# Performance work log

Measured on AMD Instinct MI355X. Metric: run time of the kernel, lower is better.

Reference implementation:

```python
import jax, jax.numpy as jnp
import numpy as np


def setup_inputs() -> dict:
    key = jax.random.key(0)
    k1, k2, k3, k4 = jax.random.split(key, 4)
    d_in, d_out = 1024, 1024
    x = jax.random.normal(k1, (4, 2048, d_in), dtype=jnp.float32)
    # nn.Linear weights, stored as [d_in, d_out] for x @ W (torch stores transpose)
    s = 1.0 / np.sqrt(d_in)
    Wq = jax.random.normal(k2, (d_in, d_out), dtype=jnp.float32) * s
    Wk = jax.random.normal(k3, (d_in, d_out), dtype=jnp.float32) * s
    Wv = jax.random.normal(k4, (d_in, d_out), dtype=jnp.float32) * s
    return {"x": x, "Wq": Wq, "Wk": Wk, "Wv": Wv}


def reference(x, Wq, Wk, Wv):
    # x: [b, s, d_in]; projections (no bias)
    q = jnp.einsum('bsi,io->bso', x, Wq)
    k = jnp.einsum('bsi,io->bso', x, Wk)
    v = jnp.einsum('bsi,io->bso', x, Wv)
    d_out = k.shape[-1]
    scores = jnp.einsum('bqd,bkd->bqk', q, k) / jnp.sqrt(jnp.float32(d_out))
    seq_len = x.shape[1]
    causal = jnp.tril(jnp.ones((seq_len, seq_len), dtype=bool))  # [s, s]
    scores = jnp.where(causal[None, :, :], scores, -jnp.inf)
    weights = jax.nn.softmax(scores, axis=-1)
    return jnp.einsum('bqk,bkd->bqd', weights, v)
```

## Files before the change

kernel.cpp:

```cpp
#include <hip/hip_runtime.h>

typedef __attribute__((ext_vector_type(8))) short bf16x8;
typedef __attribute__((ext_vector_type(4))) float f32x4;
typedef unsigned int u32;

__device__ __forceinline__ unsigned short f2bf(float f) {
  union { float f; unsigned int u; } a; a.f = f;
  unsigned int u = a.u;
  u += 0x7FFFu + ((u >> 16) & 1u);
  return (unsigned short)(u >> 16);
}

__device__ __forceinline__ void gload16(const unsigned short* g, unsigned short* l) {
  __builtin_amdgcn_global_load_lds((const __attribute__((address_space(1))) u32*)g,
                                   (__attribute__((address_space(3))) u32*)l, 16, 0, 0);
}

#define BK 64

template<int MODE>
__global__ __launch_bounds__(256, 4)
void gemm_bt(const unsigned short* __restrict__ A,
             const unsigned short* __restrict__ Bm,
             float* __restrict__ Cf,
             float* __restrict__ Cf2,
             unsigned short* __restrict__ Cb,
             int K, long aBatch, long bBatch, long cBatch, float scale)
{
  constexpr int NI    = (MODE == 0) ? 4 : 2;
  constexpr int TNc   = (MODE == 0) ? 128 : 64;
  constexpr int BROWS = (MODE == 0) ? 32 : 16;
  constexpr int BG    = (MODE == 0) ? 4 : 2;

  int z = blockIdx.z;
  A  += (long)z * aBatch;
  Bm += (long)z * bBatch;
  if (MODE == 2) { Cb += (long)z * cBatch; Cf += (long)z * 2048; }
  if (MODE == 3) { Cf += (long)z * cBatch; Cf2 += (long)z * 2048; }

  int bm0 = 0, bn, p = 0;
  if (MODE == 2) {
    int f = blockIdx.x;
    int r = (int)((sqrtf((float)(4 * f + 1)) - 1.0f) * 0.5f);
    while ((r + 1) * (r + 2) <= f) r++;
    while (r * (r + 1) > f) r--;
    bm0 = r * 128;
    bn  = (f - r * (r + 1)) * 64;
  } else if (MODE == 3) {
    p  = blockIdx.y;
    bn = blockIdx.x * 64;
  } else {
    bm0 = blockIdx.y * 128;
    bn  = blockIdx.x * TNc;
  }

  __shared__ __align__(16) unsigned short As[128 * BK];
  __shared__ __align__(16) unsigned short Bs[TNc * BK];

  int tid  = threadIdx.x;
  int wave = tid >> 6, lane = tid & 63;
  int wm = (MODE == 0) ? (wave >> 1) * 64 : wave * 32;
  int wn = (MODE == 0) ? (wave & 1) * 64 : 0;
  int quad = lane >> 4, l16 = lane & 15;

  int r8 = lane >> 3;
  int c  = (lane & 7) ^ r8;
  const unsigned short* Bg = Bm + (long)(bn + wave * BROWS + r8) * K + c * 8;
  unsigned short* Al = &As[(wave * 32) * BK];
  unsigned short* Bl = &Bs[(wave * BROWS) * BK];

  const int nseg = (MODE == 3) ? 2 : 1;
  for (int seg = 0; seg < nseg; seg++) {
    int bm   = (MODE == 3) ? ((seg == 0) ? (15 - p) * 128 : p * 128) : bm0;
    int Keff = (MODE == 3) ? ((seg == 0) ? 128 * (16 - p) : 128 * (p + 1)) : K;
    const unsigned short* Ag = A + (long)(bm + wave * 32 + r8) * K + c * 8;

    f32x4 acc[NI][4] = {};

    for (int k0 = 0; k0 < Keff; k0 += BK) {
#pragma unroll
      for (int g = 0; g < 4; g++)
        gload16(Ag + k0 + (long)g * 8 * K, Al + g * 8 * BK);
#pragma unroll
      for (int g = 0; g < BG; g++)
        gload16(Bg + k0 + (long)g * 8 * K, Bl + g * 8 * BK);
      __syncthreads();

#pragma unroll
      for (int h = 0; h < 2; h++) {
        bf16x8 af[NI], bfr[4];
#pragma unroll
        for (int i = 0; i < NI; i++)
          af[i]  = *(const bf16x8*)&As[(wm + i * 16 + l16) * BK + (((quad + 4 * h) ^ (l16 & 7)) * 8)];
#pragma unroll
        for (int j = 0; j < 4; j++)
          bfr[j] = *(const bf16x8*)&Bs[(wn + j * 16 + l16) * BK + (((quad + 4 * h) ^ (l16 & 7)) * 8)];
#pragma unroll
        for (int i = 0; i < NI; i++)
#pragma unroll
          for (int j = 0; j < 4; j++)
            acc[i][j] = __builtin_amdgcn_mfma_f32_16x16x32_bf16(af[i], bfr[j], acc[i][j], 0, 0, 0);
      }
      __syncthreads();
    }

#pragma unroll
    for (int i = 0; i < NI; i++) {
      int grow0 = bm + wm + i * 16 + quad * 4;
      if (MODE == 2) {
#pragma unroll
        for (int r = 0; r < 4; r++) {
          int grow = grow0 + r;
          float rowpart = 0.f;
#pragma unroll
          for (int j = 0; j < 4; j++) {
            int gcol = bn + j * 16 + l16;
            float e = (gcol <= grow) ? __expf(acc[i][j][r] * scale) : 0.f;
            rowpart += e;
            Cb[(long)grow * 2048 + gcol] = f2bf(e);
          }
          rowpart += __shfl_xor(rowpart, 1);
          rowpart += __shfl_xor(rowpart, 2);
          rowpart += __shfl_xor(rowpart, 4);
          rowpart += __shfl_xor(rowpart, 8);
          if (l16 == 0) atomicAdd(&Cf[grow], rowpart);
        }
      } else if (MODE == 3) {
        float rinv[4];
#pragma unroll
        for (int r = 0; r < 4; r++) rinv[r] = 1.0f / Cf2[grow0 + r];
#pragma unroll
        for (int j = 0; j < 4; j++) {
          int gcol = bn + j * 16 + l16;
#pragma unroll
          for (int r = 0; r < 4; r++)
            Cf[(long)(grow0 + r) * 1024 + gcol] = acc[i][j][r] * rinv[r];
        }
      } else if (MODE == 1) {
#pragma unroll
        for (int j = 0; j < 4; j++) {
          int gcol = bn + j * 16 + l16;
#pragma unroll
          for (int r = 0; r < 4; r++)
            Cb[(long)(grow0 + r) * 1024 + gcol] = f2bf(acc[i][j][r]);
        }
      } else {
#pragma unroll
        for (int j = 0; j < 4; j++) {
          int gcol = bn + wn + j * 16 + l16;
          int which = gcol >> 10;
          int col = gcol & 1023;
          if (which == 0) {
#pragma unroll
            for (int r = 0; r < 4; r++)
              Cb[(long)(grow0 + r) * 1024 + col] = f2bf(acc[i][j][r]);
          } else {
            unsigned short* Vt = Cb + (long)8192 * 1024;
            int bb = grow0 >> 11, s = grow0 & 2047;
            ushort4 pk;
            pk.x = f2bf(acc[i][j][0]); pk.y = f2bf(acc[i][j][1]);
            pk.z = f2bf(acc[i][j][2]); pk.w = f2bf(acc[i][j][3]);
            *(ushort4*)(Vt + ((long)bb * 1024 + col) * 2048 + s) = pk;
          }
        }
      }
    }
  }
}

__global__ __launch_bounds__(256)
void prep(const float* __restrict__ x,
          const float* __restrict__ W0, const float* __restrict__ W1,
          const float* __restrict__ W2,
          unsigned short* __restrict__ Xb,
          unsigned short* __restrict__ Wqb, unsigned short* __restrict__ Wkb,
          unsigned short* __restrict__ WvT,
          float* __restrict__ rsum)
{
  __shared__ float tile[32][33];
  int b = blockIdx.x;
  if (b < 8192) {
    long i = ((long)b * 256 + threadIdx.x) * 4;
    float4 v = *(const float4*)(x + i);
    ushort4 o;
    o.x = f2bf(v.x); o.y = f2bf(v.y); o.z = f2bf(v.z); o.w = f2bf(v.w);
    *(ushort4*)(Xb + i) = o;
  } else if (b < 10240) {
    int t = b - 8192;
    const float* W    = (t < 1024) ? W0 : W1;
    unsigned short* D = (t < 1024) ? Wqb : Wkb;
    long i = ((long)(t & 1023) * 256 + threadIdx.x) * 4;
    float4 v = *(const float4*)(W + i);
    ushort4 o;
    o.x = f2bf(v.x); o.y = f2bf(v.y); o.z = f2bf(v.z); o.w = f2bf(v.w);
    *(ushort4*)(D + i) = o;
  } else if (b < 11264) {
    int q = b - 10240;
    int kb = (q >> 5) * 32, nb = (q & 31) * 32;
    int tx = threadIdx.x & 31, ty = threadIdx.x >> 5;
    for (int r = ty; r < 32; r += 8)
      tile[r][tx] = W2[(long)(kb + r) * 1024 + nb + tx];
    __syncthreads();
    for (int r = ty; r < 32; r += 8)
      WvT[(long)(nb + r) * 1024 + kb + tx] = f2bf(tile[tx][r]);
  } else {
    long i = ((long)(b - 11264) * 256 + threadIdx.x) * 4;
    float4 zz = {0.f, 0.f, 0.f, 0.f};
    *(float4*)(rsum + i) = zz;
  }
}

extern "C" void kernel_launch(void* const* d_in, const int* in_sizes, int n_in,
                              void* d_out, int out_size, void* d_ws, size_t ws_size,
                              hipStream_t stream) {
  const float* x  = (const float*)d_in[0];
  const float* Wq = (const float*)d_in[1];
  const float* Wk = (const float*)d_in[2];
  const float* Wv = (const float*)d_in[3];
  float* out = (float*)d_out;

  unsigned short* Xb  = (unsigned short*)d_ws;
  unsigned short* Wqb = Xb  + (long)8192 * 1024;
  unsigned short* Wkb = Wqb + (long)1024 * 1024;
  unsigned short* TVB = Wkb + (long)1024 * 1024;
  unsigned short* T   = TVB + (long)2048 * 1024;
  unsigned short* Vt  = T   + (long)8192 * 1024;
  unsigned short* E   = Vt  + (long)8192 * 1024;
  float* rsum         = (float*)(E + (long)4 * 2048 * 2048);

  prep<<<11272, 256, 0, stream>>>(x, Wq, Wk, Wv, Xb, Wqb, Wkb,
                                  TVB + (long)1024 * 1024, rsum);

  gemm_bt<1><<<dim3(16, 8, 1), 256, 0, stream>>>(Wkb, Wqb, nullptr, nullptr, TVB,
      1024, 0, 0, 0, 1.f);

  gemm_bt<0><<<dim3(16, 64, 1), 256, 0, stream>>>(Xb, TVB, nullptr, nullptr, T,
      1024, 0, 0, 0, 1.f);

  gemm_bt<2><<<dim3(272, 1, 4), 256, 0, stream>>>(T, Xb, rsum, nullptr, E, 1024,
      (long)2048 * 1024, (long)2048 * 1024, (long)2048 * 2048, 0.03125f);

  gemm_bt<3><<<dim3(16, 8, 4), 256, 0, stream>>>(E, Vt, out, rsum, nullptr, 2048,
      (long)2048 * 2048, (long)1024 * 2048, (long)2048 * 1024, 1.f);
}
```

Measured before the change: 217.3 us.

## Replace projection GEMM with 256x256-tile, 4-stage pipelined 512-thread kernel

Adds a dedicated gemm_tv kernel for the X·[T|V] projection. It uses 256x256 output tiles with 8 waves, a 4-slot LDS ring of 32-wide K slices prefetched three stages ahead with global_load_lds, explicit vmcnt waits, and setprio around the MFMA block. This replaces the synchronous single-buffered 128x128 gemm_bt<0>. The goal is to hide global-load latency and raise data reuse per tile. The cost is higher register and LDS pressure and a smaller grid of 256 blocks.

```diff
diff --git a/kernel.cpp b/kernel.cpp
--- a/kernel.cpp
+++ b/kernel.cpp
@@ -163,6 +163,102 @@
             *(ushort4*)(Vt + ((long)bb * 1024 + col) * 2048 + s) = pk;
           }
         }
+      }
+    }
+  }
+}
+
+__global__ __launch_bounds__(512, 2)
+void gemm_tv(const unsigned short* __restrict__ A,
+             const unsigned short* __restrict__ Bm,
+             unsigned short* __restrict__ Cb)
+{
+  constexpr int SLICE = 32;
+  constexpr int SLOT  = 256 * SLICE;
+  __shared__ __align__(16) unsigned short As[4 * SLOT];
+  __shared__ __align__(16) unsigned short Bs[4 * SLOT];
+
+  const int tid  = threadIdx.x;
+  const int wave = tid >> 6, lane = tid & 63;
+  const int quad = lane >> 4, l16 = lane & 15;
+  const int bm = blockIdx.y * 256;
+  const int bn = blockIdx.x * 256;
+  const int wm = (wave >> 2) * 128;
+  const int wn = (wave & 3) * 64;
+
+  const int srow = lane >> 2;
+  const int sc   = ((lane & 3) ^ ((lane >> 3) & 3)) * 8;
+  const unsigned short* Ag = A  + (long)(bm + wave * 32 + srow) * 1024 + sc;
+  const unsigned short* Bg = Bm + (long)(bn + wave * 32 + srow) * 1024 + sc;
+  unsigned short* Asl = As + wave * (32 * SLICE);
+  unsigned short* Bsl = Bs + wave * (32 * SLICE);
+
+  const int pc = (quad ^ ((l16 >> 1) & 3)) * 8;
+
+  f32x4 acc[8][4] = {};
+
+#define STAGE(s)                                                          \
+  { const int so_ = ((s) & 3) * SLOT; const int ko_ = (s) * SLICE;        \
+    gload16(Ag + ko_,             Asl + so_);                             \
+    gload16(Ag + ko_ + 16 * 1024, Asl + so_ + 16 * SLICE);                \
+    gload16(Bg + ko_,             Bsl + so_);                             \
+    gload16(Bg + ko_ + 16 * 1024, Bsl + so_ + 16 * SLICE); }
+
+  STAGE(0) STAGE(1) STAGE(2)
+  asm volatile("s_waitcnt vmcnt(8) lgkmcnt(0)" ::: "memory");
+  __builtin_amdgcn_sched_barrier(0);
+  __builtin_amdgcn_s_barrier();
+
+  constexpr int ns = 1024 / SLICE;
+#pragma unroll 1
+  for (int s = 0; s < ns; ++s) {
+    if (s + 3 < ns) STAGE(s + 3)
+    const unsigned short* Asr = As + (s & 3) * SLOT;
+    const unsigned short* Bsr = Bs + (s & 3) * SLOT;
+    bf16x8 af[8], bfr[4];
+#pragma unroll
+    for (int i = 0; i < 8; ++i)
+      af[i]  = *(const bf16x8*)&Asr[(wm + i * 16 + l16) * SLICE + pc];
+#pragma unroll
+    for (int j = 0; j < 4; ++j)
+      bfr[j] = *(const bf16x8*)&Bsr[(wn + j * 16 + l16) * SLICE + pc];
+    __builtin_amdgcn_s_setprio(1);
+#pragma unroll
+    for (int i = 0; i < 8; ++i)
+#pragma unroll
+      for (int j = 0; j < 4; ++j)
+        acc[i][j] = __builtin_amdgcn_mfma_f32_16x16x32_bf16(af[i], bfr[j], acc[i][j], 0, 0, 0);
+    __builtin_amdgcn_s_setprio(0);
+    if (s < ns - 3)
+      asm volatile("s_waitcnt vmcnt(8) lgkmcnt(0)" ::: "memory");
+    else if (s == ns - 3)
+      asm volatile("s_waitcnt vmcnt(4) lgkmcnt(0)" ::: "memory");
+    else
+      asm volatile("s_waitcnt vmcnt(0) lgkmcnt(0)" ::: "memory");
+    __builtin_amdgcn_sched_barrier(0);
+    __builtin_amdgcn_s_barrier();
+  }
+#undef STAGE
+
+#pragma unroll
+  for (int i = 0; i < 8; ++i) {
+    int grow0 = bm + wm + i * 16 + quad * 4;
+#pragma unroll
+    for (int j = 0; j < 4; ++j) {
+      int gcol = bn + wn + j * 16 + l16;
+      int which = gcol >> 10;
+      int col = gcol & 1023;
+      if (which == 0) {
+#pragma unroll
+        for (int r = 0; r < 4; r++)
+          Cb[(long)(grow0 + r) * 1024 + col] = f2bf(acc[i][j][r]);
+      } else {
+        unsigned short* Vt = Cb + (long)8192 * 1024;
+        int bb = grow0 >> 11, ss = grow0 & 2047;
+        ushort4 pk;
+        pk.x = f2bf(acc[i][j][0]); pk.y = f2bf(acc[i][j][1]);
+        pk.z = f2bf(acc[i][j][2]); pk.w = f2bf(acc[i][j][3]);
+        *(ushort4*)(Vt + ((long)bb * 1024 + col) * 2048 + ss) = pk;
       }
     }
   }
@@ -234,8 +330,7 @@
   gemm_bt<1><<<dim3(16, 8, 1), 256, 0, stream>>>(Wkb, Wqb, nullptr, nullptr, TVB,
       1024, 0, 0, 0, 1.f);
 
-  gemm_bt<0><<<dim3(16, 64, 1), 256, 0, stream>>>(Xb, TVB, nullptr, nullptr, T,
-      1024, 0, 0, 0, 1.f);
+  gemm_tv<<<dim3(8, 32, 1), 512, 0, stream>>>(Xb, TVB, T);
 
   gemm_bt<2><<<dim3(272, 1, 4), 256, 0, stream>>>(T, Xb, rsum, nullptr, E, 1024,
       (long)2048 * 1024, (long)2048 * 1024, (long)2048 * 2048, 0.03125f);
```

Measured after the change: 228.3 us. +5.1%, slower.

## Replace T/V projection GEMM with 256x256 double-buffered 8-wave pipelined kernel

Applied to the files above, without the earlier changes.

The MODE 0 path of the generic GEMM, which computes x·[Wk·Wqᵀ | Wv] into T and the transposed V, is replaced by a dedicated kernel. It uses 512 threads, 256x256 output tiles and double-buffered LDS, and issues global loads for the next K-tiles while four phases of MFMAs run, with explicit vmcnt waits, barriers and setprio. The larger tile increases operand reuse per load, and the schedule is meant to hide global-load latency. In exchange it uses 128 KB of LDS per block and launches only 256 blocks, so occupancy is low and the hand-built barrier/waitcnt scheme adds correctness risk.

```diff
diff --git a/kernel.cpp b/kernel.cpp
--- a/kernel.cpp
+++ b/kernel.cpp
@@ -27,10 +27,9 @@
              unsigned short* __restrict__ Cb,
              int K, long aBatch, long bBatch, long cBatch, float scale)
 {
-  constexpr int NI    = (MODE == 0) ? 4 : 2;
-  constexpr int TNc   = (MODE == 0) ? 128 : 64;
-  constexpr int BROWS = (MODE == 0) ? 32 : 16;
-  constexpr int BG    = (MODE == 0) ? 4 : 2;
+  constexpr int NI    = 2;
+  constexpr int BROWS = 16;
+  constexpr int BG    = 2;
 
   int z = blockIdx.z;
   A  += (long)z * aBatch;
@@ -51,16 +50,15 @@
     bn = blockIdx.x * 64;
   } else {
     bm0 = blockIdx.y * 128;
-    bn  = blockIdx.x * TNc;
+    bn  = blockIdx.x * 64;
   }
 
   __shared__ __align__(16) unsigned short As[128 * BK];
-  __shared__ __align__(16) unsigned short Bs[TNc * BK];
+  __shared__ __align__(16) unsigned short Bs[64 * BK];
 
   int tid  = threadIdx.x;
   int wave = tid >> 6, lane = tid & 63;
-  int wm = (MODE == 0) ? (wave >> 1) * 64 : wave * 32;
-  int wn = (MODE == 0) ? (wave & 1) * 64 : 0;
+  int wm = wave * 32, wn = 0;
   int quad = lane >> 4, l16 = lane & 15;
 
   int r8 = lane >> 3;
@@ -136,7 +134,7 @@
           for (int r = 0; r < 4; r++)
             Cf[(long)(grow0 + r) * 1024 + gcol] = acc[i][j][r] * rinv[r];
         }
-      } else if (MODE == 1) {
+      } else {
 #pragma unroll
         for (int j = 0; j < 4; j++) {
           int gcol = bn + j * 16 + l16;
@@ -144,25 +142,127 @@
           for (int r = 0; r < 4; r++)
             Cb[(long)(grow0 + r) * 1024 + gcol] = f2bf(acc[i][j][r]);
         }
+      }
+    }
+  }
+}
+
+__global__ __launch_bounds__(512, 2)
+void gemm_tv8(const unsigned short* __restrict__ A,
+              const unsigned short* __restrict__ Bm,
+              unsigned short* __restrict__ Cb)
+{
+  constexpr int NT = 16;
+  constexpr int SLOT = 256 * 64;
+  __shared__ __align__(16) unsigned short AsL[2 * SLOT];
+  __shared__ __align__(16) unsigned short BsL[2 * SLOT];
+
+  const int tid  = threadIdx.x;
+  const int wave = tid >> 6, lane = tid & 63;
+  const int quad = lane >> 4, l16 = lane & 15;
+  const int wr = wave >> 2, wc = wave & 3;
+  const int bm = blockIdx.y * 256;
+  const int bn = blockIdx.x * 256;
+
+  const int l8 = lane >> 3;
+  const int sc = ((lane & 7) ^ l8) * 8;
+  const unsigned short* Ag = A  + (long)(bm + wave * 8 + l8) * 1024 + sc;
+  const unsigned short* Bg = Bm + (long)(bn + (wave >> 2) * 64 + (wave & 3) * 8 + l8) * 1024 + sc;
+
+#define STGA(base, h, t) {                                                      \
+    gload16(Ag + (long)((h) * 64) * 1024 + (t) * 64,        (base) + ((h) * 128 + wave * 8) * 64);      \
+    gload16(Ag + (long)(128 + (h) * 64) * 1024 + (t) * 64,  (base) + ((h) * 128 + 64 + wave * 8) * 64); }
+#define STGB(base, h, t) {                                                      \
+    gload16(Bg + (long)((h) * 32) * 1024 + (t) * 64,        (base) + ((h) * 128 + wave * 8) * 64);      \
+    gload16(Bg + (long)(128 + (h) * 32) * 1024 + (t) * 64,  (base) + ((h) * 128 + 64 + wave * 8) * 64); }
+
+#define RD_A(afX, src, qm) _Pragma("unroll") for (int i = 0; i < 4; ++i)        \
+    _Pragma("unroll") for (int h2 = 0; h2 < 2; ++h2)                            \
+      afX[i][h2] = *(const bf16x8*)&(src)[((qm) * 128 + wr * 64 + i * 16 + l16) * 64 + (((quad + 4 * h2) ^ (l16 & 7)) * 8)];
+#define RD_B(bfX, src, qn) _Pragma("unroll") for (int j = 0; j < 2; ++j)        \
+    _Pragma("unroll") for (int h2 = 0; h2 < 2; ++h2)                            \
+      bfX[j][h2] = *(const bf16x8*)&(src)[((qn) * 128 + wc * 32 + j * 16 + l16) * 64 + (((quad + 4 * h2) ^ (l16 & 7)) * 8)];
+#define MFMA16(afX, bfX, MI0, NJ0) {                                            \
+    __builtin_amdgcn_s_setprio(1);                                              \
+    _Pragma("unroll") for (int i = 0; i < 4; ++i)                               \
+      _Pragma("unroll") for (int j = 0; j < 2; ++j)                             \
+        _Pragma("unroll") for (int h2 = 0; h2 < 2; ++h2)                        \
+          acc[(MI0) + i][(NJ0) + j] =                                           \
+            __builtin_amdgcn_mfma_f32_16x16x32_bf16(afX[i][h2], bfX[j][h2], acc[(MI0) + i][(NJ0) + j], 0, 0, 0); \
+    __builtin_amdgcn_s_setprio(0); }
+
+  f32x4 acc[8][4] = {};
+
+  STGA(AsL, 0, 0) STGB(BsL, 0, 0)
+  STGA(AsL, 1, 0) STGB(BsL, 1, 0)
+  STGB(BsL + SLOT, 0, 1) STGA(AsL + SLOT, 1, 1)
+  asm volatile("s_waitcnt vmcnt(4)" ::: "memory");
+  __builtin_amdgcn_sched_barrier(0);
+  __builtin_amdgcn_s_barrier();
+
+#pragma unroll 1
+  for (int u = 0; u < NT; ++u) {
+    const int b = u & 1;
+    const unsigned short* Asb = AsL + b * SLOT;
+    const unsigned short* Bsb = BsL + b * SLOT;
+    unsigned short* Asn = AsL + (b ^ 1) * SLOT;
+    unsigned short* Bsn = BsL + (b ^ 1) * SLOT;
+    unsigned short* Asc = AsL + b * SLOT;
+    unsigned short* Bsc = BsL + b * SLOT;
+
+    bf16x8 af0[4][2], af1[4][2], bf0[2][2], bf1[2][2];
+
+    RD_A(af0, Asb, 0)
+    RD_B(bf0, Bsb, 0)
+    if (u + 1 < NT) { STGA(Asn, 0, u + 1) STGB(Bsn, 1, u + 1) }
+    __builtin_amdgcn_s_barrier();
+    MFMA16(af0, bf0, 0, 0)
+    __builtin_amdgcn_s_barrier();
+
+    RD_A(af1, Asb, 1)
+    if (u + 2 < NT) STGB(Bsc, 0, u + 2)
+    __builtin_amdgcn_s_barrier();
+    MFMA16(af1, bf0, 4, 0)
+    __builtin_amdgcn_s_barrier();
+
+    RD_B(bf1, Bsb, 1)
+    if (u + 2 < NT) STGA(Asc, 1, u + 2)
+    __builtin_amdgcn_s_barrier();
+    MFMA16(af1, bf1, 4, 2)
+    __builtin_amdgcn_s_barrier();
+
+    if (u < NT - 2)       { asm volatile("s_waitcnt vmcnt(4)" ::: "memory"); }
+    else if (u == NT - 2) { asm volatile("s_waitcnt vmcnt(0)" ::: "memory"); }
+    __builtin_amdgcn_sched_barrier(0);
+    __builtin_amdgcn_s_barrier();
+    MFMA16(af0, bf1, 0, 2)
+    __builtin_amdgcn_s_barrier();
+  }
+#undef STGA
+#undef STGB
+#undef RD_A
+#undef RD_B
+#undef MFMA16
+
+#pragma unroll
+  for (int mi = 0; mi < 8; ++mi) {
+    int grow0 = bm + wr * 128 + mi * 16 + quad * 4;
+#pragma unroll
+    for (int nj = 0; nj < 4; ++nj) {
+      int gcol = bn + wc * 64 + nj * 16 + l16;
+      int which = gcol >> 10;
+      int col = gcol & 1023;
+      if (which == 0) {
+#pragma unroll
+        for (int r = 0; r < 4; r++)
+          Cb[(long)(grow0 + r) * 1024 + col] = f2bf(acc[mi][nj][r]);
       } else {
-#pragma unroll
-        for (int j = 0; j < 4; j++) {
-          int gcol = bn + wn + j * 16 + l16;
-          int which = gcol >> 10;
-          int col = gcol & 1023;
-          if (which == 0) {
-#pragma unroll
-            for (int r = 0; r < 4; r++)
-              Cb[(long)(grow0 + r) * 1024 + col] = f2bf(acc[i][j][r]);
-          } else {
-            unsigned short* Vt = Cb + (long)8192 * 1024;
-            int bb = grow0 >> 11, s = grow0 & 2047;
-            ushort4 pk;
-            pk.x = f2bf(acc[i][j][0]); pk.y = f2bf(acc[i][j][1]);
-            pk.z = f2bf(acc[i][j][2]); pk.w = f2bf(acc[i][j][3]);
-            *(ushort4*)(Vt + ((long)bb * 1024 + col) * 2048 + s) = pk;
-          }
-        }
+        unsigned short* Vt = Cb + (long)8192 * 1024;
+        int bb = grow0 >> 11, s = grow0 & 2047;
+        ushort4 pk;
+        pk.x = f2bf(acc[mi][nj][0]); pk.y = f2bf(acc[mi][nj][1]);
+        pk.z = f2bf(acc[mi][nj][2]); pk.w = f2bf(acc[mi][nj][3]);
+        *(ushort4*)(Vt + ((long)bb * 1024 + col) * 2048 + s) = pk;
       }
     }
   }
@@ -234,8 +334,7 @@
   gemm_bt<1><<<dim3(16, 8, 1), 256, 0, stream>>>(Wkb, Wqb, nullptr, nullptr, TVB,
       1024, 0, 0, 0, 1.f);
 
-  gemm_bt<0><<<dim3(16, 64, 1), 256, 0, stream>>>(Xb, TVB, nullptr, nullptr, T,
-      1024, 0, 0, 0, 1.f);
+  gemm_tv8<<<dim3(8, 32, 1), 512, 0, stream>>>(Xb, TVB, T);
 
   gemm_bt<2><<<dim3(272, 1, 4), 256, 0, stream>>>(T, Xb, rsum, nullptr, E, 1024,
       (long)2048 * 1024, (long)2048 * 1024, (long)2048 * 2048, 0.03125f);
```

Result: no change. 217.1 us (-0.1%).
